# Performance work log

Measured on AMD Instinct MI355X. Metric: run time of the kernel, lower is better.

Reference implementation:

```python
import jax, jax.numpy as jnp
import numpy as np

B, S, D, F, E, TOP_K = 2, 2048, 1024, 2048, 8, 2


def setup_inputs() -> dict:
    key = jax.random.key(0)
    k0, k1, k2, k3 = jax.random.split(key, 4)
    return {
        "hidden_states": jax.random.normal(k0, (B, S, D), jnp.float32),
        "gate_w": jax.random.normal(k1, (E, D), jnp.float32) * 0.02,   # torch Linear weight [out=E, in=D]
        "w1": jax.random.normal(k2, (E, D, F), jnp.float32) * 0.02,    # per-expert up-proj
        "w2": jax.random.normal(k3, (E, F, D), jnp.float32) * 0.02,    # per-expert down-proj
    }


def reference(hidden_states, gate_w, w1, w2):
    b, s, d = hidden_states.shape
    e = gate_w.shape[0]
    x = hidden_states.reshape(-1, d)                 # [T, D]
    t = x.shape[0]
    router_logits = x @ gate_w.T                     # [T, E]
    # softmax in fp32 as in original, then renormalized top-k weights
    probs = jax.nn.softmax(router_logits.astype(jnp.float32), axis=-1)
    topw, sel = jax.lax.top_k(probs, TOP_K)          # [T, K]
    topw = topw / jnp.sum(topw, axis=-1, keepdims=True)
    topw = topw.astype(x.dtype)
    # dense combine weights: zero for unselected experts (top_k indices are distinct)
    combine = jnp.zeros((t, e), x.dtype).at[jnp.arange(t)[:, None], sel].add(topw)  # [T, E]
    out = jnp.zeros_like(x)
    for ei in range(e):  # small fixed expert count
        h = jax.nn.silu(x @ w1[ei]) @ w2[ei]         # [T, D]
        out = out + combine[:, ei:ei + 1] * h
    return out.reshape(b, s, d), router_logits
```

## Files before the change

### kernel.cpp

```cpp
#include <hip/hip_runtime.h>
#include <hip/hip_bf16.h>
#include <math.h>

#define Tt 4096
#define Dd 1024
#define Ff 2048
#define Ee 8

typedef unsigned short u16;
typedef short bf16x8 __attribute__((ext_vector_type(8)));
typedef float f32x4 __attribute__((ext_vector_type(4)));

__device__ __forceinline__ u16 f2bf(float f) {
  union { float f; unsigned u; } v; v.f = f;
  unsigned r = v.u + 0x7fffu + ((v.u >> 16) & 1u);
  return (u16)(r >> 16);
}

__device__ __forceinline__ void gload16(const void* g, void* l) {
  __builtin_amdgcn_global_load_lds(
      (const __attribute__((address_space(1))) unsigned int*)g,
      (__attribute__((address_space(3))) unsigned int*)l, 16, 0, 0);
}

__global__ __launch_bounds__(256) void router_kernel(
    const float* __restrict__ x, const float* __restrict__ gw,
    float* __restrict__ logits, u16* __restrict__ xb)
{
  int t = blockIdx.x * 4 + (threadIdx.x >> 6);
  int lane = threadIdx.x & 63;
  const float* xr = x + (size_t)t * Dd;
  float xv[16];
#pragma unroll
  for (int i = 0; i < 4; ++i) {
    float4 v = *reinterpret_cast<const float4*>(xr + lane * 16 + i * 4);
    xv[i*4+0] = v.x; xv[i*4+1] = v.y; xv[i*4+2] = v.z; xv[i*4+3] = v.w;
  }
  if (xb) {
#pragma unroll
    for (int i = 0; i < 4; ++i) {
      ushort4 b;
      b.x = f2bf(xv[i*4+0]); b.y = f2bf(xv[i*4+1]);
      b.z = f2bf(xv[i*4+2]); b.w = f2bf(xv[i*4+3]);
      *reinterpret_cast<ushort4*>(xb + (size_t)t * Dd + lane * 16 + i * 4) = b;
    }
  }
#pragma unroll
  for (int e = 0; e < Ee; ++e) {
    const float* gr = gw + (size_t)e * Dd + lane * 16;
    float s = 0.f;
#pragma unroll
    for (int i = 0; i < 4; ++i) {
      float4 g = *reinterpret_cast<const float4*>(gr + i * 4);
      s += xv[i*4+0]*g.x + xv[i*4+1]*g.y + xv[i*4+2]*g.z + xv[i*4+3]*g.w;
    }
#pragma unroll
    for (int o = 32; o > 0; o >>= 1) s += __shfl_xor(s, o);
    if (lane == 0) logits[(size_t)t * Ee + e] = s;
  }
}

__global__ __launch_bounds__(256) void build_kernel(
    const float* __restrict__ logits, int* __restrict__ meta,
    int* __restrict__ list, float* __restrict__ wgt)
{
  __shared__ int hist[8], cur[8];
  const int tid = threadIdx.x;
  const int lane = tid & 63;
  if (tid < 8) hist[tid] = 0;
  __syncthreads();
  for (int it = 0; it < Tt / 256; ++it) {
    int t = it * 256 + tid;
    float4 lo = *reinterpret_cast<const float4*>(logits + (size_t)t * 8);
    float4 hi = *reinterpret_cast<const float4*>(logits + (size_t)t * 8 + 4);
    float s[8] = {lo.x, lo.y, lo.z, lo.w, hi.x, hi.y, hi.z, hi.w};
    int i1 = 0; float m1 = s[0];
#pragma unroll
    for (int e = 1; e < 8; ++e) if (s[e] > m1) { m1 = s[e]; i1 = e; }
    int i2 = -1; float m2 = -__builtin_inff();
#pragma unroll
    for (int e = 0; e < 8; ++e) if (e != i1 && s[e] > m2) { m2 = s[e]; i2 = e; }
#pragma unroll
    for (int k = 0; k < 2; ++k) {
      int gg = k ? i2 : i1;
      unsigned long long m = ~0ull;
#pragma unroll
      for (int b = 0; b < 3; ++b) {
        unsigned long long vb = __ballot((gg >> b) & 1);
        m &= ((gg >> b) & 1) ? vb : ~vb;
      }
      int rank = __popcll(m & ((1ull << lane) - 1));
      if (rank == 0) atomicAdd(&hist[gg], __popcll(m));
    }
  }
  __syncthreads();
  if (tid == 0) {
    int sacc = 0;
    for (int g = 0; g < 8; ++g) {
      meta[g] = hist[g];
      meta[32 + g] = sacc;
      cur[g] = sacc;
      sacc += hist[g];
    }
  }
  __syncthreads();
  for (int it = 0; it < Tt / 256; ++it) {
    int t = it * 256 + tid;
    float4 lo = *reinterpret_cast<const float4*>(logits + (size_t)t * 8);
    float4 hi = *reinterpret_cast<const float4*>(logits + (size_t)t * 8 + 4);
    float s[8] = {lo.x, lo.y, lo.z, lo.w, hi.x, hi.y, hi.z, hi.w};
    int i1 = 0; float m1 = s[0];
#pragma unroll
    for (int e = 1; e < 8; ++e) if (s[e] > m1) { m1 = s[e]; i1 = e; }
    int i2 = -1; float m2 = -__builtin_inff();
#pragma unroll
    for (int e = 0; e < 8; ++e) if (e != i1 && s[e] > m2) { m2 = s[e]; i2 = e; }
    float wa = 1.f / (1.f + expf(m2 - m1));
#pragma unroll
    for (int k = 0; k < 2; ++k) {
      int gg = k ? i2 : i1;
      float w = k ? (1.f - wa) : wa;
      unsigned long long m = ~0ull;
#pragma unroll
      for (int b = 0; b < 3; ++b) {
        unsigned long long vb = __ballot((gg >> b) & 1);
        m &= ((gg >> b) & 1) ? vb : ~vb;
      }
      int rank = __popcll(m & ((1ull << lane) - 1));
      int ldr = __ffsll(m) - 1;
      int base = 0;
      if (rank == 0) base = atomicAdd(&cur[gg], __popcll(m));
      base = __shfl(base, ldr);
      list[base + rank] = t;
      wgt[base + rank] = w;
    }
  }
}

__global__ __launch_bounds__(256) void transpose_bf16_kernel(
    const float* __restrict__ in, u16* __restrict__ out, int R, int C)
{
  __shared__ u16 st[64][65];
  const size_t eoff = (size_t)blockIdx.z * R * C;
  const float* ip = in + eoff;
  u16* op = out + eoff;
  int r0 = blockIdx.y * 64, c0 = blockIdx.x * 64;
  int t = threadIdx.x;
  int rr = t >> 2;
  int cb = (t & 3) * 16;
#pragma unroll
  for (int i = 0; i < 4; ++i) {
    float4 v = *reinterpret_cast<const float4*>(ip + (size_t)(r0 + rr) * C + c0 + cb + i * 4);
    st[rr][cb + i*4 + 0] = f2bf(v.x);
    st[rr][cb + i*4 + 1] = f2bf(v.y);
    st[rr][cb + i*4 + 2] = f2bf(v.z);
    st[rr][cb + i*4 + 3] = f2bf(v.w);
  }
  __syncthreads();
#pragma unroll
  for (int i = 0; i < 4; ++i) {
    ushort4 b;
    b.x = st[cb + i*4 + 0][rr];
    b.y = st[cb + i*4 + 1][rr];
    b.z = st[cb + i*4 + 2][rr];
    b.w = st[cb + i*4 + 3][rr];
    *reinterpret_cast<ushort4*>(op + (size_t)(c0 + rr) * R + r0 + cb + i * 4) = b;
  }
}

template<int MODE, int N_, int K_>
__global__ __launch_bounds__(256) void gemm_g(
    const u16* __restrict__ Abase, const u16* __restrict__ Bbase,
    void* __restrict__ Cout, const int* __restrict__ meta,
    const int* __restrict__ list, const float* __restrict__ wgt)
{
  constexpr int NXc = N_ / 128;
  constexpr int NYc = 32;
  constexpr int CPX = NXc * NYc;
  constexpr int ABUF = 128 * 32;
  constexpr int NT  = K_ / 32;

  __shared__ u16 Al[3 * ABUF];
  __shared__ u16 Bl[3 * ABUF];

  const int orig = blockIdx.x + NXc * (blockIdx.y + NYc * blockIdx.z);
  const int swz  = (orig & 7) * CPX + (orig >> 3);
  const int bz   = swz / (NXc * NYc);
  const int rem  = swz - bz * (NXc * NYc);
  const int by   = rem / NXc;
  const int bx   = rem - by * NXc;

  const int e   = bz;
  const int cnt = meta[e];
  if (by * 128 >= cnt) return;
  const int off = meta[32 + e];

  const int tid  = threadIdx.x;
  const int lane = tid & 63;
  const int wave = tid >> 6;
  const int wr   = wave >> 1, wc = wave & 1;
  const int n0   = bx * 128;

  const int l4 = lane >> 2;
  const int kp = (((lane & 3) ^ ((lane >> 3) & 3))) * 8;

  const u16* aptr[2];
  int aoff[2];
#pragma unroll
  for (int c = 0; c < 2; ++c) {
    int chunk = wave * 2 + c;
    int row = chunk * 16 + l4;
    int i = by * 128 + row;
    if (i >= cnt) i = cnt - 1;
    int srow = (MODE == 0) ? list[off + i] : (off + i);
    aptr[c] = Abase + (size_t)srow * K_ + kp;
    aoff[c] = chunk * 512;
  }
  const u16* bptr[2];
  int boff[2];
#pragma unroll
  for (int c = 0; c < 2; ++c) {
    int chunk = wave * 2 + c;
    int row = chunk * 16 + l4;
    bptr[c] = Bbase + ((size_t)e * N_ + n0 + row) * K_ + kp;
    boff[c] = chunk * 512;
  }

  f32x4 acc[4][4] = {};
  const int r16 = lane & 15;
  const int kqs = (((lane >> 4) ^ ((lane >> 1) & 3))) * 8;

  u16 *a0 = Al, *a1 = Al + ABUF, *a2 = Al + 2 * ABUF;
  u16 *b0 = Bl, *b1 = Bl + ABUF, *b2 = Bl + 2 * ABUF;

#pragma unroll
  for (int c = 0; c < 2; ++c) { gload16(aptr[c], a0 + aoff[c]); gload16(bptr[c], b0 + boff[c]); }
#pragma unroll
  for (int c = 0; c < 2; ++c) { gload16(aptr[c] + 32, a1 + aoff[c]); gload16(bptr[c] + 32, b1 + boff[c]); }

  for (int t = 0; t < NT; ++t) {
    if (t + 1 < NT) asm volatile("s_waitcnt vmcnt(4)" ::: "memory");
    else            asm volatile("s_waitcnt vmcnt(0)" ::: "memory");
    __builtin_amdgcn_s_barrier();

    if (t + 2 < NT) {
      int k0 = (t + 2) * 32;
#pragma unroll
      for (int c = 0; c < 2; ++c) { gload16(aptr[c] + k0, a2 + aoff[c]); gload16(bptr[c] + k0, b2 + boff[c]); }
    }

    bf16x8 af[4], bfv[4];
#pragma unroll
    for (int m = 0; m < 4; ++m)
      af[m] = *reinterpret_cast<const bf16x8*>(&a0[(wr*64 + m*16 + r16) * 32 + kqs]);
#pragma unroll
    for (int n = 0; n < 4; ++n)
      bfv[n] = *reinterpret_cast<const bf16x8*>(&b0[(wc*64 + n*16 + r16) * 32 + kqs]);
    __builtin_amdgcn_s_setprio(1);
#pragma unroll
    for (int m = 0; m < 4; ++m)
#pragma unroll
      for (int n = 0; n < 4; ++n)
        acc[m][n] = __builtin_amdgcn_mfma_f32_16x16x32_bf16(af[m], bfv[n], acc[m][n], 0, 0, 0);
    __builtin_amdgcn_s_setprio(0);

    u16* ta = a0; a0 = a1; a1 = a2; a2 = ta;
    u16* tb = b0; b0 = b1; b1 = b2; b2 = tb;
  }

  const int colb = n0 + wc * 64 + r16;
  const int rb4  = wr * 64 + ((lane >> 4) << 2);
#pragma unroll
  for (int m = 0; m < 4; ++m) {
#pragma unroll
    for (int r = 0; r < 4; ++r) {
      int i = by * 128 + rb4 + m * 16 + r;
      if (i >= cnt) continue;
      if (MODE == 0) {
        u16* hp = (u16*)Cout + (size_t)(off + i) * N_;
#pragma unroll
        for (int n = 0; n < 4; ++n) {
          float v = acc[m][n][r];
          v = v / (1.f + expf(-v));
          hp[colb + n * 16] = f2bf(v);
        }
      } else {
        int   tok = list[off + i];
        float w   = wgt[off + i];
        float* o = (float*)Cout + (size_t)tok * N_;
#pragma unroll
        for (int n = 0; n < 4; ++n)
          atomicAdd(&o[colb + n * 16], w * acc[m][n][r]);
      }
    }
  }
}

__global__ __launch_bounds__(256) void combine_kernel(
    const float* __restrict__ logits, float* __restrict__ combine)
{
  int t = blockIdx.x * 256 + threadIdx.x;
  if (t >= Tt) return;
  float4 lo = *reinterpret_cast<const float4*>(logits + (size_t)t * 8);
  float4 hi = *reinterpret_cast<const float4*>(logits + (size_t)t * 8 + 4);
  float s[8] = {lo.x, lo.y, lo.z, lo.w, hi.x, hi.y, hi.z, hi.w};
  int i1 = 0; float m1 = s[0];
#pragma unroll
  for (int e = 1; e < 8; ++e) if (s[e] > m1) { m1 = s[e]; i1 = e; }
  int i2 = -1; float m2 = -__builtin_inff();
#pragma unroll
  for (int e = 0; e < 8; ++e) if (e != i1 && s[e] > m2) { m2 = s[e]; i2 = e; }
  float wa = 1.f / (1.f + expf(m2 - m1));
#pragma unroll
  for (int e = 0; e < 8; ++e)
    combine[(size_t)t * 8 + e] = (e == i1) ? wa : ((e == i2) ? (1.f - wa) : 0.f);
}

template<int MODE, int N_, int K_>
__global__ __launch_bounds__(256) void gemm_dense(
    const float* __restrict__ A, const float* __restrict__ Bg,
    float* __restrict__ C, const float* __restrict__ combine,
    int expert, int first)
{
  constexpr int BM = 128, BN = 128, BK = 32, LDT = 40;
  __shared__ u16 Al[BM * LDT];
  __shared__ u16 Bl[BN * LDT];
  const int tid  = threadIdx.x;
  const int lane = tid & 63;
  const int wave = tid >> 6;
  const int wr = wave >> 1, wc = wave & 1;
  const int m0 = blockIdx.y * BM;
  const int n0 = blockIdx.x * BN;
  f32x4 acc[4][4] = {};
  for (int k0 = 0; k0 < K_; k0 += BK) {
#pragma unroll
    for (int i = 0; i < 4; ++i) {
      int f = tid + 256 * i;
      int row = f >> 3;
      int c4 = (f & 7) << 2;
      float4 v = *reinterpret_cast<const float4*>(A + (size_t)(m0 + row) * K_ + k0 + c4);
      ushort4 b;
      b.x = f2bf(v.x); b.y = f2bf(v.y); b.z = f2bf(v.z); b.w = f2bf(v.w);
      *reinterpret_cast<ushort4*>(&Al[row * LDT + c4]) = b;
    }
    {
      int n  = tid & 127;
      int kb = (tid >> 7) << 4;
      const float* bp = Bg + (size_t)(k0 + kb) * N_ + n0 + n;
      u16 tmp[16];
#pragma unroll
      for (int kk = 0; kk < 16; ++kk)
        tmp[kk] = f2bf(bp[(size_t)kk * N_]);
      u16* p = &Bl[n * LDT + kb];
#pragma unroll
      for (int i = 0; i < 4; ++i) {
        ushort4 b;
        b.x = tmp[i*4+0]; b.y = tmp[i*4+1]; b.z = tmp[i*4+2]; b.w = tmp[i*4+3];
        *reinterpret_cast<ushort4*>(p + i * 4) = b;
      }
    }
    __syncthreads();
    bf16x8 af[4], bfr[4];
    const int kq  = (lane >> 4) << 3;
    const int r16 = lane & 15;
#pragma unroll
    for (int m = 0; m < 4; ++m)
      af[m] = *reinterpret_cast<const bf16x8*>(&Al[(wr*64 + m*16 + r16) * LDT + kq]);
#pragma unroll
    for (int n = 0; n < 4; ++n)
      bfr[n] = *reinterpret_cast<const bf16x8*>(&Bl[(wc*64 + n*16 + r16) * LDT + kq]);
#pragma unroll
    for (int m = 0; m < 4; ++m)
#pragma unroll
      for (int n = 0; n < 4; ++n)
        acc[m][n] = __builtin_amdgcn_mfma_f32_16x16x32_bf16(af[m], bfr[n], acc[m][n], 0, 0, 0);
    __syncthreads();
  }
  const int col0 = n0 + wc * 64 + (lane & 15);
  const int rbs  = m0 + wr * 64 + ((lane >> 4) << 2);
#pragma unroll
  for (int m = 0; m < 4; ++m) {
#pragma unroll
    for (int r = 0; r < 4; ++r) {
      int row = rbs + m * 16 + r;
      if (MODE == 0) {
#pragma unroll
        for (int n = 0; n < 4; ++n) {
          float v = acc[m][n][r];
          v = v / (1.f + expf(-v));
          C[(size_t)row * N_ + col0 + n * 16] = v;
        }
      } else {
        float w = combine[(size_t)row * Ee + expert];
        if (first) {
#pragma unroll
          for (int n = 0; n < 4; ++n)
            C[(size_t)row * N_ + col0 + n * 16] = w * acc[m][n][r];
        } else {
#pragma unroll
          for (int n = 0; n < 4; ++n)
            C[(size_t)row * N_ + col0 + n * 16] += w * acc[m][n][r];
        }
      }
    }
  }
}

extern "C" void kernel_launch(void* const* d_in, const int* in_sizes, int n_in,
                              void* d_out, int out_size, void* d_ws, size_t ws_size,
                              hipStream_t stream)
{
  const float* x  = (const float*)d_in[0];
  const float* gw = (const float*)d_in[1];
  const float* w1 = (const float*)d_in[2];
  const float* w2 = (const float*)d_in[3];
  float* out    = (float*)d_out;
  float* logits = out + (size_t)Tt * Dd;

  int*   meta = (int*)d_ws;
  int*   list = (int*)((char*)d_ws + 256);
  float* wgt  = (float*)((char*)d_ws + 256 + 32768);
  u16*   xb   = (u16*)((char*)d_ws + 262144);
  u16*   h1   = (u16*)((char*)d_ws + 262144 + 8388608);
  u16*   wT   = (u16*)((char*)d_ws + 262144 + 8388608 + 33554432);
  const size_t NEED = 262144ull + 8388608ull + 33554432ull + 33554432ull;

  if (ws_size >= NEED) {
    router_kernel<<<Tt / 4, 256, 0, stream>>>(x, gw, logits, xb);
    hipMemsetAsync(out, 0, (size_t)Tt * Dd * sizeof(float), stream);
    build_kernel<<<1, 256, 0, stream>>>(logits, meta, list, wgt);
    transpose_bf16_kernel<<<dim3(Ff/64, Dd/64, Ee), 256, 0, stream>>>(w1, wT, Dd, Ff);
    gemm_g<0, Ff, Dd><<<dim3(Ff/128, 32, 8), 256, 0, stream>>>(xb, wT, h1, meta, list, wgt);
    transpose_bf16_kernel<<<dim3(Dd/64, Ff/64, Ee), 256, 0, stream>>>(w2, wT, Ff, Dd);
    gemm_g<1, Dd, Ff><<<dim3(Dd/128, 32, 8), 256, 0, stream>>>(h1, wT, out, meta, list, wgt);
  } else {
    float* combine = (float*)d_ws;
    float* h1d     = combine + (size_t)Tt * Ee;
    router_kernel<<<Tt / 4, 256, 0, stream>>>(x, gw, logits, nullptr);
    combine_kernel<<<Tt / 256, 256, 0, stream>>>(logits, combine);
    size_t cb = (size_t)Tt * Ee * sizeof(float);
    size_t avail = ws_size > cb ? (ws_size - cb) : 0;
    long maxrows = (long)(avail / ((size_t)Ff * sizeof(float)));
    int chunk = (maxrows >= Tt) ? Tt : (int)((maxrows / 128) * 128);
    if (chunk < 128) chunk = 128;
    for (int c0 = 0; c0 < Tt; c0 += chunk) {
      int rows = (Tt - c0) < chunk ? (Tt - c0) : chunk;
      for (int e = 0; e < Ee; ++e) {
        gemm_dense<0, Ff, Dd><<<dim3(Ff/128, rows/128), 256, 0, stream>>>(
            x + (size_t)c0 * Dd, w1 + (size_t)e * Dd * Ff, h1d, nullptr, e, 0);
        gemm_dense<1, Dd, Ff><<<dim3(Dd/128, rows/128), 256, 0, stream>>>(
            h1d, w2 + (size_t)e * Ff * Dd, out + (size_t)c0 * Dd,
            combine + (size_t)c0 * Ee, e, (e == 0) ? 1 : 0);
      }
    }
  }
}
```

Before: 207.2 us.

## Enlarge grouped GEMM tile to 256x128 and split-K the down-projection

The grouped expert GEMMs now use a 256-row by 128-column block tile, with each wave covering 64 rows across all 128 columns, so B tiles are reused over more rows and fewer blocks are launched. The down-projection GEMM also splits K in two, with each half atomically accumulating into the output, to restore the parallelism lost from the larger tile. The accumulator grows to 4x8 per wave under a 2-blocks-per-CU launch bound, which raises register pressure and LDS use. The split doubles the fp32 atomic traffic on the output.

```diff
diff --git a/kernel.cpp b/kernel.cpp
--- a/kernel.cpp
+++ b/kernel.cpp
@@ -168,20 +168,23 @@
   }
 }
 
-template<int MODE, int N_, int K_>
-__global__ __launch_bounds__(256) void gemm_g(
+template<int MODE, int N_, int K_, int KSPLIT>
+__global__ __launch_bounds__(256, 2) void gemm_g(
     const u16* __restrict__ Abase, const u16* __restrict__ Bbase,
     void* __restrict__ Cout, const int* __restrict__ meta,
     const int* __restrict__ list, const float* __restrict__ wgt)
 {
+  constexpr int BM  = 256;
   constexpr int NXc = N_ / 128;
-  constexpr int NYc = 32;
-  constexpr int CPX = NXc * NYc;
-  constexpr int ABUF = 128 * 32;
-  constexpr int NT  = K_ / 32;
+  constexpr int NYc = 16;
+  constexpr int CPX = NXc * NYc * KSPLIT;
+  constexpr int ABUF = BM * 32;
+  constexpr int BBUF = 128 * 32;
+  constexpr int KLOC = K_ / KSPLIT;
+  constexpr int NT  = KLOC / 32;
 
   __shared__ u16 Al[3 * ABUF];
-  __shared__ u16 Bl[3 * ABUF];
+  __shared__ u16 Bl[3 * BBUF];
 
   const int orig = blockIdx.x + NXc * (blockIdx.y + NYc * blockIdx.z);
   const int swz  = (orig & 7) * CPX + (orig >> 3);
@@ -190,77 +193,84 @@
   const int by   = rem / NXc;
   const int bx   = rem - by * NXc;
 
-  const int e   = bz;
+  const int e   = bz / KSPLIT;
+  const int kh  = bz - e * KSPLIT;
   const int cnt = meta[e];
-  if (by * 128 >= cnt) return;
+  if (by * BM >= cnt) return;
   const int off = meta[32 + e];
+  const int kbase = kh * KLOC;
 
   const int tid  = threadIdx.x;
   const int lane = tid & 63;
   const int wave = tid >> 6;
-  const int wr   = wave >> 1, wc = wave & 1;
   const int n0   = bx * 128;
 
   const int l4 = lane >> 2;
   const int kp = (((lane & 3) ^ ((lane >> 3) & 3))) * 8;
 
-  const u16* aptr[2];
-  int aoff[2];
+  const u16* aptr[4];
+  int aoff[4];
+#pragma unroll
+  for (int c = 0; c < 4; ++c) {
+    int chunk = wave * 4 + c;
+    int rw = chunk * 16 + l4;
+    int i = by * BM + rw;
+    if (i >= cnt) i = cnt - 1;
+    int srow = (MODE == 0) ? list[off + i] : (off + i);
+    aptr[c] = Abase + (size_t)srow * K_ + kbase + kp;
+    aoff[c] = chunk * 512;
+  }
+  const u16* bptr[2];
+  int boff[2];
 #pragma unroll
   for (int c = 0; c < 2; ++c) {
     int chunk = wave * 2 + c;
-    int row = chunk * 16 + l4;
-    int i = by * 128 + row;
-    if (i >= cnt) i = cnt - 1;
-    int srow = (MODE == 0) ? list[off + i] : (off + i);
-    aptr[c] = Abase + (size_t)srow * K_ + kp;
-    aoff[c] = chunk * 512;
-  }
-  const u16* bptr[2];
-  int boff[2];
-#pragma unroll
-  for (int c = 0; c < 2; ++c) {
-    int chunk = wave * 2 + c;
-    int row = chunk * 16 + l4;
-    bptr[c] = Bbase + ((size_t)e * N_ + n0 + row) * K_ + kp;
+    int rw = chunk * 16 + l4;
+    bptr[c] = Bbase + ((size_t)e * N_ + n0 + rw) * K_ + kbase + kp;
     boff[c] = chunk * 512;
   }
 
-  f32x4 acc[4][4] = {};
+  f32x4 acc[4][8] = {};
   const int r16 = lane & 15;
   const int kqs = (((lane >> 4) ^ ((lane >> 1) & 3))) * 8;
 
   u16 *a0 = Al, *a1 = Al + ABUF, *a2 = Al + 2 * ABUF;
-  u16 *b0 = Bl, *b1 = Bl + ABUF, *b2 = Bl + 2 * ABUF;
-
-#pragma unroll
-  for (int c = 0; c < 2; ++c) { gload16(aptr[c], a0 + aoff[c]); gload16(bptr[c], b0 + boff[c]); }
-#pragma unroll
-  for (int c = 0; c < 2; ++c) { gload16(aptr[c] + 32, a1 + aoff[c]); gload16(bptr[c] + 32, b1 + boff[c]); }
+  u16 *b0 = Bl, *b1 = Bl + BBUF, *b2 = Bl + 2 * BBUF;
+
+#pragma unroll
+  for (int c = 0; c < 4; ++c) gload16(aptr[c], a0 + aoff[c]);
+#pragma unroll
+  for (int c = 0; c < 2; ++c) gload16(bptr[c], b0 + boff[c]);
+#pragma unroll
+  for (int c = 0; c < 4; ++c) gload16(aptr[c] + 32, a1 + aoff[c]);
+#pragma unroll
+  for (int c = 0; c < 2; ++c) gload16(bptr[c] + 32, b1 + boff[c]);
 
   for (int t = 0; t < NT; ++t) {
-    if (t + 1 < NT) asm volatile("s_waitcnt vmcnt(4)" ::: "memory");
+    if (t + 1 < NT) asm volatile("s_waitcnt vmcnt(6)" ::: "memory");
     else            asm volatile("s_waitcnt vmcnt(0)" ::: "memory");
     __builtin_amdgcn_s_barrier();
 
     if (t + 2 < NT) {
       int k0 = (t + 2) * 32;
 #pragma unroll
-      for (int c = 0; c < 2; ++c) { gload16(aptr[c] + k0, a2 + aoff[c]); gload16(bptr[c] + k0, b2 + boff[c]); }
-    }
-
-    bf16x8 af[4], bfv[4];
+      for (int c = 0; c < 4; ++c) gload16(aptr[c] + k0, a2 + aoff[c]);
+#pragma unroll
+      for (int c = 0; c < 2; ++c) gload16(bptr[c] + k0, b2 + boff[c]);
+    }
+
+    bf16x8 af[4], bfv[8];
 #pragma unroll
     for (int m = 0; m < 4; ++m)
-      af[m] = *reinterpret_cast<const bf16x8*>(&a0[(wr*64 + m*16 + r16) * 32 + kqs]);
-#pragma unroll
-    for (int n = 0; n < 4; ++n)
-      bfv[n] = *reinterpret_cast<const bf16x8*>(&b0[(wc*64 + n*16 + r16) * 32 + kqs]);
+      af[m] = *reinterpret_cast<const bf16x8*>(&a0[(wave*64 + m*16 + r16) * 32 + kqs]);
+#pragma unroll
+    for (int n = 0; n < 8; ++n)
+      bfv[n] = *reinterpret_cast<const bf16x8*>(&b0[(n*16 + r16) * 32 + kqs]);
     __builtin_amdgcn_s_setprio(1);
 #pragma unroll
     for (int m = 0; m < 4; ++m)
 #pragma unroll
-      for (int n = 0; n < 4; ++n)
+      for (int n = 0; n < 8; ++n)
         acc[m][n] = __builtin_amdgcn_mfma_f32_16x16x32_bf16(af[m], bfv[n], acc[m][n], 0, 0, 0);
     __builtin_amdgcn_s_setprio(0);
 
@@ -268,29 +278,28 @@
     u16* tb = b0; b0 = b1; b1 = b2; b2 = tb;
   }
 
-  const int colb = n0 + wc * 64 + r16;
-  const int rb4  = wr * 64 + ((lane >> 4) << 2);
+  const int rb4 = wave * 64 + ((lane >> 4) << 2);
 #pragma unroll
   for (int m = 0; m < 4; ++m) {
 #pragma unroll
     for (int r = 0; r < 4; ++r) {
-      int i = by * 128 + rb4 + m * 16 + r;
+      int i = by * BM + rb4 + m * 16 + r;
       if (i >= cnt) continue;
       if (MODE == 0) {
         u16* hp = (u16*)Cout + (size_t)(off + i) * N_;
 #pragma unroll
-        for (int n = 0; n < 4; ++n) {
+        for (int n = 0; n < 8; ++n) {
           float v = acc[m][n][r];
           v = v / (1.f + expf(-v));
-          hp[colb + n * 16] = f2bf(v);
+          hp[n0 + n * 16 + r16] = f2bf(v);
         }
       } else {
         int   tok = list[off + i];
         float w   = wgt[off + i];
         float* o = (float*)Cout + (size_t)tok * N_;
 #pragma unroll
-        for (int n = 0; n < 4; ++n)
-          atomicAdd(&o[colb + n * 16], w * acc[m][n][r]);
+        for (int n = 0; n < 8; ++n)
+          atomicAdd(&o[n0 + n * 16 + r16], w * acc[m][n][r]);
       }
     }
   }
@@ -430,9 +439,9 @@
     hipMemsetAsync(out, 0, (size_t)Tt * Dd * sizeof(float), stream);
     build_kernel<<<1, 256, 0, stream>>>(logits, meta, list, wgt);
     transpose_bf16_kernel<<<dim3(Ff/64, Dd/64, Ee), 256, 0, stream>>>(w1, wT, Dd, Ff);
-    gemm_g<0, Ff, Dd><<<dim3(Ff/128, 32, 8), 256, 0, stream>>>(xb, wT, h1, meta, list, wgt);
+    gemm_g<0, Ff, Dd, 1><<<dim3(Ff/128, 16, 8), 256, 0, stream>>>(xb, wT, h1, meta, list, wgt);
     transpose_bf16_kernel<<<dim3(Dd/64, Ff/64, Ee), 256, 0, stream>>>(w2, wT, Ff, Dd);
-    gemm_g<1, Dd, Ff><<<dim3(Dd/128, 32, 8), 256, 0, stream>>>(h1, wT, out, meta, list, wgt);
+    gemm_g<1, Dd, Ff, 2><<<dim3(Dd/128, 16, 16), 256, 0, stream>>>(h1, wT, out, meta, list, wgt);
   } else {
     float* combine = (float*)d_ws;
     float* h1d     = combine + (size_t)Tt * Ee;
```

New measurement: 253.5 us. +22.3%, slower.

## Make grouped MoE GEMM persistent over row tiles and swizzle transpose blocks

Applied to the files above, without the earlier changes.

The grouped expert GEMMs now launch 12 row-tile slots per expert instead of 32. Each block loops over row tiles with a stride of 12 until it has covered that expert's token count, with a barrier between tiles so the shared-memory buffers can be reused. Most of the 32 row slots in the old grid returned immediately, so this cuts launch overhead and empty blocks, but large experts become serial within a block. The weight transpose kernel also gets the same XCD-style block-index swizzle used by the GEMM, to spread experts across dies.

```diff
diff --git a/kernel.cpp b/kernel.cpp
--- a/kernel.cpp
+++ b/kernel.cpp
@@ -141,10 +141,20 @@
     const float* __restrict__ in, u16* __restrict__ out, int R, int C)
 {
   __shared__ u16 st[64][65];
-  const size_t eoff = (size_t)blockIdx.z * R * C;
+  const int gx = gridDim.x, gy = gridDim.y;
+  const int plane = gx * gy;
+  const int cpx = plane;
+  const int orig = blockIdx.x + gx * (blockIdx.y + gy * blockIdx.z);
+  const int swz  = (orig & 7) * cpx + (orig >> 3);
+  const int ez   = swz / plane;
+  const int rem  = swz - ez * plane;
+  const int byy  = rem / gx;
+  const int bxx  = rem - byy * gx;
+
+  const size_t eoff = (size_t)ez * R * C;
   const float* ip = in + eoff;
   u16* op = out + eoff;
-  int r0 = blockIdx.y * 64, c0 = blockIdx.x * 64;
+  int r0 = byy * 64, c0 = bxx * 64;
   int t = threadIdx.x;
   int rr = t >> 2;
   int cb = (t & 3) * 16;
@@ -175,7 +185,7 @@
     const int* __restrict__ list, const float* __restrict__ wgt)
 {
   constexpr int NXc = N_ / 128;
-  constexpr int NYc = 32;
+  constexpr int NYc = 12;
   constexpr int CPX = NXc * NYc;
   constexpr int ABUF = 128 * 32;
   constexpr int NT  = K_ / 32;
@@ -185,14 +195,13 @@
 
   const int orig = blockIdx.x + NXc * (blockIdx.y + NYc * blockIdx.z);
   const int swz  = (orig & 7) * CPX + (orig >> 3);
-  const int bz   = swz / (NXc * NYc);
-  const int rem  = swz - bz * (NXc * NYc);
-  const int by   = rem / NXc;
-  const int bx   = rem - by * NXc;
+  const int bz   = swz / CPX;
+  const int rem  = swz - bz * CPX;
+  const int by0  = rem / NXc;
+  const int bx   = rem - by0 * NXc;
 
   const int e   = bz;
   const int cnt = meta[e];
-  if (by * 128 >= cnt) return;
   const int off = meta[32 + e];
 
   const int tid  = threadIdx.x;
@@ -203,96 +212,98 @@
 
   const int l4 = lane >> 2;
   const int kp = (((lane & 3) ^ ((lane >> 3) & 3))) * 8;
-
-  const u16* aptr[2];
-  int aoff[2];
-#pragma unroll
-  for (int c = 0; c < 2; ++c) {
-    int chunk = wave * 2 + c;
-    int row = chunk * 16 + l4;
-    int i = by * 128 + row;
-    if (i >= cnt) i = cnt - 1;
-    int srow = (MODE == 0) ? list[off + i] : (off + i);
-    aptr[c] = Abase + (size_t)srow * K_ + kp;
-    aoff[c] = chunk * 512;
-  }
-  const u16* bptr[2];
-  int boff[2];
-#pragma unroll
-  for (int c = 0; c < 2; ++c) {
-    int chunk = wave * 2 + c;
-    int row = chunk * 16 + l4;
-    bptr[c] = Bbase + ((size_t)e * N_ + n0 + row) * K_ + kp;
-    boff[c] = chunk * 512;
-  }
-
-  f32x4 acc[4][4] = {};
   const int r16 = lane & 15;
   const int kqs = (((lane >> 4) ^ ((lane >> 1) & 3))) * 8;
 
-  u16 *a0 = Al, *a1 = Al + ABUF, *a2 = Al + 2 * ABUF;
-  u16 *b0 = Bl, *b1 = Bl + ABUF, *b2 = Bl + 2 * ABUF;
-
-#pragma unroll
-  for (int c = 0; c < 2; ++c) { gload16(aptr[c], a0 + aoff[c]); gload16(bptr[c], b0 + boff[c]); }
-#pragma unroll
-  for (int c = 0; c < 2; ++c) { gload16(aptr[c] + 32, a1 + aoff[c]); gload16(bptr[c] + 32, b1 + boff[c]); }
-
-  for (int t = 0; t < NT; ++t) {
-    if (t + 1 < NT) asm volatile("s_waitcnt vmcnt(4)" ::: "memory");
-    else            asm volatile("s_waitcnt vmcnt(0)" ::: "memory");
-    __builtin_amdgcn_s_barrier();
-
-    if (t + 2 < NT) {
-      int k0 = (t + 2) * 32;
-#pragma unroll
-      for (int c = 0; c < 2; ++c) { gload16(aptr[c] + k0, a2 + aoff[c]); gload16(bptr[c] + k0, b2 + boff[c]); }
-    }
-
-    bf16x8 af[4], bfv[4];
-#pragma unroll
-    for (int m = 0; m < 4; ++m)
-      af[m] = *reinterpret_cast<const bf16x8*>(&a0[(wr*64 + m*16 + r16) * 32 + kqs]);
-#pragma unroll
-    for (int n = 0; n < 4; ++n)
-      bfv[n] = *reinterpret_cast<const bf16x8*>(&b0[(wc*64 + n*16 + r16) * 32 + kqs]);
-    __builtin_amdgcn_s_setprio(1);
-#pragma unroll
-    for (int m = 0; m < 4; ++m)
+  for (int by = by0; by * 128 < cnt; by += NYc) {
+    const u16* aptr[2];
+    int aoff[2];
+#pragma unroll
+    for (int c = 0; c < 2; ++c) {
+      int chunk = wave * 2 + c;
+      int rw = chunk * 16 + l4;
+      int i = by * 128 + rw;
+      if (i >= cnt) i = cnt - 1;
+      int srow = (MODE == 0) ? list[off + i] : (off + i);
+      aptr[c] = Abase + (size_t)srow * K_ + kp;
+      aoff[c] = chunk * 512;
+    }
+    const u16* bptr[2];
+    int boff[2];
+#pragma unroll
+    for (int c = 0; c < 2; ++c) {
+      int chunk = wave * 2 + c;
+      int rw = chunk * 16 + l4;
+      bptr[c] = Bbase + ((size_t)e * N_ + n0 + rw) * K_ + kp;
+      boff[c] = chunk * 512;
+    }
+
+    f32x4 acc[4][4] = {};
+    u16 *a0 = Al, *a1 = Al + ABUF, *a2 = Al + 2 * ABUF;
+    u16 *b0 = Bl, *b1 = Bl + ABUF, *b2 = Bl + 2 * ABUF;
+
+#pragma unroll
+    for (int c = 0; c < 2; ++c) { gload16(aptr[c], a0 + aoff[c]); gload16(bptr[c], b0 + boff[c]); }
+#pragma unroll
+    for (int c = 0; c < 2; ++c) { gload16(aptr[c] + 32, a1 + aoff[c]); gload16(bptr[c] + 32, b1 + boff[c]); }
+
+    for (int t = 0; t < NT; ++t) {
+      if (t + 1 < NT) asm volatile("s_waitcnt vmcnt(4)" ::: "memory");
+      else            asm volatile("s_waitcnt vmcnt(0)" ::: "memory");
+      __builtin_amdgcn_s_barrier();
+
+      if (t + 2 < NT) {
+        int k0 = (t + 2) * 32;
+#pragma unroll
+        for (int c = 0; c < 2; ++c) { gload16(aptr[c] + k0, a2 + aoff[c]); gload16(bptr[c] + k0, b2 + boff[c]); }
+      }
+
+      bf16x8 af[4], bfv[4];
+#pragma unroll
+      for (int m = 0; m < 4; ++m)
+        af[m] = *reinterpret_cast<const bf16x8*>(&a0[(wr*64 + m*16 + r16) * 32 + kqs]);
 #pragma unroll
       for (int n = 0; n < 4; ++n)
-        acc[m][n] = __builtin_amdgcn_mfma_f32_16x16x32_bf16(af[m], bfv[n], acc[m][n], 0, 0, 0);
-    __builtin_amdgcn_s_setprio(0);
-
-    u16* ta = a0; a0 = a1; a1 = a2; a2 = ta;
-    u16* tb = b0; b0 = b1; b1 = b2; b2 = tb;
-  }
-
-  const int colb = n0 + wc * 64 + r16;
-  const int rb4  = wr * 64 + ((lane >> 4) << 2);
-#pragma unroll
-  for (int m = 0; m < 4; ++m) {
-#pragma unroll
-    for (int r = 0; r < 4; ++r) {
-      int i = by * 128 + rb4 + m * 16 + r;
-      if (i >= cnt) continue;
-      if (MODE == 0) {
-        u16* hp = (u16*)Cout + (size_t)(off + i) * N_;
-#pragma unroll
-        for (int n = 0; n < 4; ++n) {
-          float v = acc[m][n][r];
-          v = v / (1.f + expf(-v));
-          hp[colb + n * 16] = f2bf(v);
+        bfv[n] = *reinterpret_cast<const bf16x8*>(&b0[(wc*64 + n*16 + r16) * 32 + kqs]);
+      __builtin_amdgcn_s_setprio(1);
+#pragma unroll
+      for (int m = 0; m < 4; ++m)
+#pragma unroll
+        for (int n = 0; n < 4; ++n)
+          acc[m][n] = __builtin_amdgcn_mfma_f32_16x16x32_bf16(af[m], bfv[n], acc[m][n], 0, 0, 0);
+      __builtin_amdgcn_s_setprio(0);
+
+      u16* ta = a0; a0 = a1; a1 = a2; a2 = ta;
+      u16* tb = b0; b0 = b1; b1 = b2; b2 = tb;
+    }
+
+    const int colb = n0 + wc * 64 + r16;
+    const int rb4  = wr * 64 + ((lane >> 4) << 2);
+#pragma unroll
+    for (int m = 0; m < 4; ++m) {
+#pragma unroll
+      for (int r = 0; r < 4; ++r) {
+        int i = by * 128 + rb4 + m * 16 + r;
+        if (i >= cnt) continue;
+        if (MODE == 0) {
+          u16* hp = (u16*)Cout + (size_t)(off + i) * N_;
+#pragma unroll
+          for (int n = 0; n < 4; ++n) {
+            float v = acc[m][n][r];
+            v = v / (1.f + expf(-v));
+            hp[colb + n * 16] = f2bf(v);
+          }
+        } else {
+          int   tok = list[off + i];
+          float w   = wgt[off + i];
+          float* o = (float*)Cout + (size_t)tok * N_;
+#pragma unroll
+          for (int n = 0; n < 4; ++n)
+            atomicAdd(&o[colb + n * 16], w * acc[m][n][r]);
         }
-      } else {
-        int   tok = list[off + i];
-        float w   = wgt[off + i];
-        float* o = (float*)Cout + (size_t)tok * N_;
-#pragma unroll
-        for (int n = 0; n < 4; ++n)
-          atomicAdd(&o[colb + n * 16], w * acc[m][n][r]);
-      }
-    }
+      }
+    }
+    __syncthreads();
   }
 }
 
@@ -430,9 +441,9 @@
     hipMemsetAsync(out, 0, (size_t)Tt * Dd * sizeof(float), stream);
     build_kernel<<<1, 256, 0, stream>>>(logits, meta, list, wgt);
     transpose_bf16_kernel<<<dim3(Ff/64, Dd/64, Ee), 256, 0, stream>>>(w1, wT, Dd, Ff);
-    gemm_g<0, Ff, Dd><<<dim3(Ff/128, 32, 8), 256, 0, stream>>>(xb, wT, h1, meta, list, wgt);
+    gemm_g<0, Ff, Dd><<<dim3(Ff/128, 12, 8), 256, 0, stream>>>(xb, wT, h1, meta, list, wgt);
     transpose_bf16_kernel<<<dim3(Dd/64, Ff/64, Ee), 256, 0, stream>>>(w2, wT, Ff, Dd);
-    gemm_g<1, Dd, Ff><<<dim3(Dd/128, 32, 8), 256, 0, stream>>>(h1, wT, out, meta, list, wgt);
+    gemm_g<1, Dd, Ff><<<dim3(Dd/128, 12, 8), 256, 0, stream>>>(h1, wT, out, meta, list, wgt);
   } else {
     float* combine = (float*)d_ws;
     float* h1d     = combine + (size_t)Tt * Ee;
```

Result: slower. 282.9 us (+36.5%).

## Fuse router with w1 transpose and overlap w2 transpose with first GEMM

Applied to the files above, without the earlier changes.

Merges the router and the w1 fp32-to-bf16 transpose into one launch of heterogeneous blocks. It also merges the first grouped GEMM with the w2 transpose, using a separate workspace buffer so both can run concurrently. This is meant to cut launch gaps and fill idle CUs: many first-GEMM blocks exit early because of per-expert token counts, and transpose blocks can occupy those CUs. The cost is an extra 32MB of workspace, and the fused GEMM kernel's LDS footprint applies to the transpose blocks too. If the workspace is too small, it falls back to the old sequence.

```diff
diff --git a/kernel.cpp b/kernel.cpp
--- a/kernel.cpp
+++ b/kernel.cpp
@@ -23,12 +23,11 @@
       (__attribute__((address_space(3))) unsigned int*)l, 16, 0, 0);
 }
 
-__global__ __launch_bounds__(256) void router_kernel(
-    const float* __restrict__ x, const float* __restrict__ gw,
+__device__ __forceinline__ void router_body(
+    int t, int tid, const float* __restrict__ x, const float* __restrict__ gw,
     float* __restrict__ logits, u16* __restrict__ xb)
 {
-  int t = blockIdx.x * 4 + (threadIdx.x >> 6);
-  int lane = threadIdx.x & 63;
+  int lane = tid & 63;
   const float* xr = x + (size_t)t * Dd;
   float xv[16];
 #pragma unroll
@@ -58,6 +57,228 @@
     for (int o = 32; o > 0; o >>= 1) s += __shfl_xor(s, o);
     if (lane == 0) logits[(size_t)t * Ee + e] = s;
   }
+}
+
+__device__ __forceinline__ void transpose_tile(
+    const float* __restrict__ ip, u16* __restrict__ op, int R, int C,
+    int r0, int c0, int tid, u16 st[][65])
+{
+  int rr = tid >> 2;
+  int cb = (tid & 3) * 16;
+#pragma unroll
+  for (int i = 0; i < 4; ++i) {
+    float4 v = *reinterpret_cast<const float4*>(ip + (size_t)(r0 + rr) * C + c0 + cb + i * 4);
+    st[rr][cb + i*4 + 0] = f2bf(v.x);
+    st[rr][cb + i*4 + 1] = f2bf(v.y);
+    st[rr][cb + i*4 + 2] = f2bf(v.z);
+    st[rr][cb + i*4 + 3] = f2bf(v.w);
+  }
+  __syncthreads();
+#pragma unroll
+  for (int i = 0; i < 4; ++i) {
+    ushort4 b;
+    b.x = st[cb + i*4 + 0][rr];
+    b.y = st[cb + i*4 + 1][rr];
+    b.z = st[cb + i*4 + 2][rr];
+    b.w = st[cb + i*4 + 3][rr];
+    *reinterpret_cast<ushort4*>(op + (size_t)(c0 + rr) * R + r0 + cb + i * 4) = b;
+  }
+}
+
+template<int MODE, int N_, int K_>
+__device__ __forceinline__ void gemm_body(
+    int orig, u16* __restrict__ Al, u16* __restrict__ Bl,
+    const u16* __restrict__ Abase, const u16* __restrict__ Bbase,
+    void* __restrict__ Cout, const int* __restrict__ meta,
+    const int* __restrict__ list, const float* __restrict__ wgt)
+{
+  constexpr int NXc = N_ / 128;
+  constexpr int NYc = 32;
+  constexpr int CPX = NXc * NYc;
+  constexpr int ABUF = 128 * 32;
+  constexpr int NT  = K_ / 32;
+
+  const int swz  = (orig & 7) * CPX + (orig >> 3);
+  const int bz   = swz / CPX;
+  const int rem  = swz - bz * CPX;
+  const int by   = rem / NXc;
+  const int bx   = rem - by * NXc;
+
+  const int e   = bz;
+  const int cnt = meta[e];
+  if (by * 128 >= cnt) return;
+  const int off = meta[32 + e];
+
+  const int tid  = threadIdx.x;
+  const int lane = tid & 63;
+  const int wave = tid >> 6;
+  const int wr   = wave >> 1, wc = wave & 1;
+  const int n0   = bx * 128;
+
+  const int l4 = lane >> 2;
+  const int kp = (((lane & 3) ^ ((lane >> 3) & 3))) * 8;
+
+  const u16* aptr[2];
+  int aoff[2];
+#pragma unroll
+  for (int c = 0; c < 2; ++c) {
+    int chunk = wave * 2 + c;
+    int row = chunk * 16 + l4;
+    int i = by * 128 + row;
+    if (i >= cnt) i = cnt - 1;
+    int srow = (MODE == 0) ? list[off + i] : (off + i);
+    aptr[c] = Abase + (size_t)srow * K_ + kp;
+    aoff[c] = chunk * 512;
+  }
+  const u16* bptr[2];
+  int boff[2];
+#pragma unroll
+  for (int c = 0; c < 2; ++c) {
+    int chunk = wave * 2 + c;
+    int row = chunk * 16 + l4;
+    bptr[c] = Bbase + ((size_t)e * N_ + n0 + row) * K_ + kp;
+    boff[c] = chunk * 512;
+  }
+
+  f32x4 acc[4][4] = {};
+  const int r16 = lane & 15;
+  const int kqs = (((lane >> 4) ^ ((lane >> 1) & 3))) * 8;
+
+  u16 *a0 = Al, *a1 = Al + ABUF, *a2 = Al + 2 * ABUF;
+  u16 *b0 = Bl, *b1 = Bl + ABUF, *b2 = Bl + 2 * ABUF;
+
+#pragma unroll
+  for (int c = 0; c < 2; ++c) { gload16(aptr[c], a0 + aoff[c]); gload16(bptr[c], b0 + boff[c]); }
+#pragma unroll
+  for (int c = 0; c < 2; ++c) { gload16(aptr[c] + 32, a1 + aoff[c]); gload16(bptr[c] + 32, b1 + boff[c]); }
+
+  for (int t = 0; t < NT; ++t) {
+    if (t + 1 < NT) asm volatile("s_waitcnt vmcnt(4)" ::: "memory");
+    else            asm volatile("s_waitcnt vmcnt(0)" ::: "memory");
+    __builtin_amdgcn_s_barrier();
+
+    if (t + 2 < NT) {
+      int k0 = (t + 2) * 32;
+#pragma unroll
+      for (int c = 0; c < 2; ++c) { gload16(aptr[c] + k0, a2 + aoff[c]); gload16(bptr[c] + k0, b2 + boff[c]); }
+    }
+
+    bf16x8 af[4], bfv[4];
+#pragma unroll
+    for (int m = 0; m < 4; ++m)
+      af[m] = *reinterpret_cast<const bf16x8*>(&a0[(wr*64 + m*16 + r16) * 32 + kqs]);
+#pragma unroll
+    for (int n = 0; n < 4; ++n)
+      bfv[n] = *reinterpret_cast<const bf16x8*>(&b0[(wc*64 + n*16 + r16) * 32 + kqs]);
+    __builtin_amdgcn_s_setprio(1);
+#pragma unroll
+    for (int m = 0; m < 4; ++m)
+#pragma unroll
+      for (int n = 0; n < 4; ++n)
+        acc[m][n] = __builtin_amdgcn_mfma_f32_16x16x32_bf16(af[m], bfv[n], acc[m][n], 0, 0, 0);
+    __builtin_amdgcn_s_setprio(0);
+
+    u16* ta = a0; a0 = a1; a1 = a2; a2 = ta;
+    u16* tb = b0; b0 = b1; b1 = b2; b2 = tb;
+  }
+
+  const int colb = n0 + wc * 64 + r16;
+  const int rb4  = wr * 64 + ((lane >> 4) << 2);
+#pragma unroll
+  for (int m = 0; m < 4; ++m) {
+#pragma unroll
+    for (int r = 0; r < 4; ++r) {
+      int i = by * 128 + rb4 + m * 16 + r;
+      if (i >= cnt) continue;
+      if (MODE == 0) {
+        u16* hp = (u16*)Cout + (size_t)(off + i) * N_;
+#pragma unroll
+        for (int n = 0; n < 4; ++n) {
+          float v = acc[m][n][r];
+          v = v / (1.f + expf(-v));
+          hp[colb + n * 16] = f2bf(v);
+        }
+      } else {
+        int   tok = list[off + i];
+        float w   = wgt[off + i];
+        float* o = (float*)Cout + (size_t)tok * N_;
+#pragma unroll
+        for (int n = 0; n < 4; ++n)
+          atomicAdd(&o[colb + n * 16], w * acc[m][n][r]);
+      }
+    }
+  }
+}
+
+__global__ __launch_bounds__(256) void router_kernel(
+    const float* __restrict__ x, const float* __restrict__ gw,
+    float* __restrict__ logits, u16* __restrict__ xb)
+{
+  router_body(blockIdx.x * 4 + (threadIdx.x >> 6), threadIdx.x, x, gw, logits, xb);
+}
+
+__global__ __launch_bounds__(256) void fuse1_kernel(
+    const float* __restrict__ x, const float* __restrict__ gw,
+    float* __restrict__ logits, u16* __restrict__ xb,
+    const float* __restrict__ w1, u16* __restrict__ w1T)
+{
+  __shared__ u16 st[64][65];
+  const int orig = blockIdx.x;
+  if (orig < 4096) {
+    int swz = (orig & 7) * 512 + (orig >> 3);
+    int e   = swz / 512;
+    int rem = swz - e * 512;
+    int by  = rem / 32, bx = rem - (rem / 32) * 32;
+    const size_t eo = (size_t)e * Dd * Ff;
+    transpose_tile(w1 + eo, w1T + eo, Dd, Ff, by * 64, bx * 64, threadIdx.x, st);
+  } else {
+    router_body((orig - 4096) * 4 + (threadIdx.x >> 6), threadIdx.x, x, gw, logits, xb);
+  }
+}
+
+__global__ __launch_bounds__(256) void fuse2_kernel(
+    const u16* __restrict__ Abase, const u16* __restrict__ Bbase,
+    void* __restrict__ Cout, const int* __restrict__ meta,
+    const int* __restrict__ list, const float* __restrict__ wgt,
+    const float* __restrict__ w2, u16* __restrict__ w2T)
+{
+  constexpr int ABUF = 128 * 32;
+  __shared__ u16 pool[6 * ABUF];
+  const int orig = blockIdx.x;
+  if (orig < 4096) {
+    gemm_body<0, Ff, Dd>(orig, pool, pool + 3 * ABUF, Abase, Bbase, Cout, meta, list, wgt);
+  } else {
+    int og  = orig - 4096;
+    int swz = (og & 7) * 512 + (og >> 3);
+    int e   = swz / 512;
+    int rem = swz - e * 512;
+    int byy = rem / 16, bxx = rem - (rem / 16) * 16;
+    const size_t eo = (size_t)e * Ff * Dd;
+    transpose_tile(w2 + eo, w2T + eo, Ff, Dd, byy * 64, bxx * 64, threadIdx.x,
+                   reinterpret_cast<u16(*)[65]>(pool));
+  }
+}
+
+template<int MODE, int N_, int K_>
+__global__ __launch_bounds__(256) void gemm_g(
+    const u16* __restrict__ Abase, const u16* __restrict__ Bbase,
+    void* __restrict__ Cout, const int* __restrict__ meta,
+    const int* __restrict__ list, const float* __restrict__ wgt)
+{
+  constexpr int ABUF = 128 * 32;
+  __shared__ u16 Al[3 * ABUF];
+  __shared__ u16 Bl[3 * ABUF];
+  const int orig = blockIdx.x + (N_ / 128) * (blockIdx.y + 32 * blockIdx.z);
+  gemm_body<MODE, N_, K_>(orig, Al, Bl, Abase, Bbase, Cout, meta, list, wgt);
+}
+
+__global__ __launch_bounds__(256) void transpose_bf16_kernel(
+    const float* __restrict__ in, u16* __restrict__ out, int R, int C)
+{
+  __shared__ u16 st[64][65];
+  const size_t eoff = (size_t)blockIdx.z * R * C;
+  transpose_tile(in + eoff, out + eoff, R, C, blockIdx.y * 64, blockIdx.x * 64,
+                 threadIdx.x, st);
 }
 
 __global__ __launch_bounds__(256) void build_kernel(
@@ -137,165 +358,6 @@
   }
 }
 
-__global__ __launch_bounds__(256) void transpose_bf16_kernel(
-    const float* __restrict__ in, u16* __restrict__ out, int R, int C)
-{
-  __shared__ u16 st[64][65];
-  const size_t eoff = (size_t)blockIdx.z * R * C;
-  const float* ip = in + eoff;
-  u16* op = out + eoff;
-  int r0 = blockIdx.y * 64, c0 = blockIdx.x * 64;
-  int t = threadIdx.x;
-  int rr = t >> 2;
-  int cb = (t & 3) * 16;
-#pragma unroll
-  for (int i = 0; i < 4; ++i) {
-    float4 v = *reinterpret_cast<const float4*>(ip + (size_t)(r0 + rr) * C + c0 + cb + i * 4);
-    st[rr][cb + i*4 + 0] = f2bf(v.x);
-    st[rr][cb + i*4 + 1] = f2bf(v.y);
-    st[rr][cb + i*4 + 2] = f2bf(v.z);
-    st[rr][cb + i*4 + 3] = f2bf(v.w);
-  }
-  __syncthreads();
-#pragma unroll
-  for (int i = 0; i < 4; ++i) {
-    ushort4 b;
-    b.x = st[cb + i*4 + 0][rr];
-    b.y = st[cb + i*4 + 1][rr];
-    b.z = st[cb + i*4 + 2][rr];
-    b.w = st[cb + i*4 + 3][rr];
-    *reinterpret_cast<ushort4*>(op + (size_t)(c0 + rr) * R + r0 + cb + i * 4) = b;
-  }
-}
-
-template<int MODE, int N_, int K_>
-__global__ __launch_bounds__(256) void gemm_g(
-    const u16* __restrict__ Abase, const u16* __restrict__ Bbase,
-    void* __restrict__ Cout, const int* __restrict__ meta,
-    const int* __restrict__ list, const float* __restrict__ wgt)
-{
-  constexpr int NXc = N_ / 128;
-  constexpr int NYc = 32;
-  constexpr int CPX = NXc * NYc;
-  constexpr int ABUF = 128 * 32;
-  constexpr int NT  = K_ / 32;
-
-  __shared__ u16 Al[3 * ABUF];
-  __shared__ u16 Bl[3 * ABUF];
-
-  const int orig = blockIdx.x + NXc * (blockIdx.y + NYc * blockIdx.z);
-  const int swz  = (orig & 7) * CPX + (orig >> 3);
-  const int bz   = swz / (NXc * NYc);
-  const int rem  = swz - bz * (NXc * NYc);
-  const int by   = rem / NXc;
-  const int bx   = rem - by * NXc;
-
-  const int e   = bz;
-  const int cnt = meta[e];
-  if (by * 128 >= cnt) return;
-  const int off = meta[32 + e];
-
-  const int tid  = threadIdx.x;
-  const int lane = tid & 63;
-  const int wave = tid >> 6;
-  const int wr   = wave >> 1, wc = wave & 1;
-  const int n0   = bx * 128;
-
-  const int l4 = lane >> 2;
-  const int kp = (((lane & 3) ^ ((lane >> 3) & 3))) * 8;
-
-  const u16* aptr[2];
-  int aoff[2];
-#pragma unroll
-  for (int c = 0; c < 2; ++c) {
-    int chunk = wave * 2 + c;
-    int row = chunk * 16 + l4;
-    int i = by * 128 + row;
-    if (i >= cnt) i = cnt - 1;
-    int srow = (MODE == 0) ? list[off + i] : (off + i);
-    aptr[c] = Abase + (size_t)srow * K_ + kp;
-    aoff[c] = chunk * 512;
-  }
-  const u16* bptr[2];
-  int boff[2];
-#pragma unroll
-  for (int c = 0; c < 2; ++c) {
-    int chunk = wave * 2 + c;
-    int row = chunk * 16 + l4;
-    bptr[c] = Bbase + ((size_t)e * N_ + n0 + row) * K_ + kp;
-    boff[c] = chunk * 512;
-  }
-
-  f32x4 acc[4][4] = {};
-  const int r16 = lane & 15;
-  const int kqs = (((lane >> 4) ^ ((lane >> 1) & 3))) * 8;
-
-  u16 *a0 = Al, *a1 = Al + ABUF, *a2 = Al + 2 * ABUF;
-  u16 *b0 = Bl, *b1 = Bl + ABUF, *b2 = Bl + 2 * ABUF;
-
-#pragma unroll
-  for (int c = 0; c < 2; ++c) { gload16(aptr[c], a0 + aoff[c]); gload16(bptr[c], b0 + boff[c]); }
-#pragma unroll
-  for (int c = 0; c < 2; ++c) { gload16(aptr[c] + 32, a1 + aoff[c]); gload16(bptr[c] + 32, b1 + boff[c]); }
-
-  for (int t = 0; t < NT; ++t) {
-    if (t + 1 < NT) asm volatile("s_waitcnt vmcnt(4)" ::: "memory");
-    else            asm volatile("s_waitcnt vmcnt(0)" ::: "memory");
-    __builtin_amdgcn_s_barrier();
-
-    if (t + 2 < NT) {
-      int k0 = (t + 2) * 32;
-#pragma unroll
-      for (int c = 0; c < 2; ++c) { gload16(aptr[c] + k0, a2 + aoff[c]); gload16(bptr[c] + k0, b2 + boff[c]); }
-    }
-
-    bf16x8 af[4], bfv[4];
-#pragma unroll
-    for (int m = 0; m < 4; ++m)
-      af[m] = *reinterpret_cast<const bf16x8*>(&a0[(wr*64 + m*16 + r16) * 32 + kqs]);
-#pragma unroll
-    for (int n = 0; n < 4; ++n)
-      bfv[n] = *reinterpret_cast<const bf16x8*>(&b0[(wc*64 + n*16 + r16) * 32 + kqs]);
-    __builtin_amdgcn_s_setprio(1);
-#pragma unroll
-    for (int m = 0; m < 4; ++m)
-#pragma unroll
-      for (int n = 0; n < 4; ++n)
-        acc[m][n] = __builtin_amdgcn_mfma_f32_16x16x32_bf16(af[m], bfv[n], acc[m][n], 0, 0, 0);
-    __builtin_amdgcn_s_setprio(0);
-
-    u16* ta = a0; a0 = a1; a1 = a2; a2 = ta;
-    u16* tb = b0; b0 = b1; b1 = b2; b2 = tb;
-  }
-
-  const int colb = n0 + wc * 64 + r16;
-  const int rb4  = wr * 64 + ((lane >> 4) << 2);
-#pragma unroll
-  for (int m = 0; m < 4; ++m) {
-#pragma unroll
-    for (int r = 0; r < 4; ++r) {
-      int i = by * 128 + rb4 + m * 16 + r;
-      if (i >= cnt) continue;
-      if (MODE == 0) {
-        u16* hp = (u16*)Cout + (size_t)(off + i) * N_;
-#pragma unroll
-        for (int n = 0; n < 4; ++n) {
-          float v = acc[m][n][r];
-          v = v / (1.f + expf(-v));
-          hp[colb + n * 16] = f2bf(v);
-        }
-      } else {
-        int   tok = list[off + i];
-        float w   = wgt[off + i];
-        float* o = (float*)Cout + (size_t)tok * N_;
-#pragma unroll
-        for (int n = 0; n < 4; ++n)
-          atomicAdd(&o[colb + n * 16], w * acc[m][n][r]);
-      }
-    }
-  }
-}
-
 __global__ __launch_bounds__(256) void combine_kernel(
     const float* __restrict__ logits, float* __restrict__ combine)
 {
@@ -422,17 +484,23 @@
   float* wgt  = (float*)((char*)d_ws + 256 + 32768);
   u16*   xb   = (u16*)((char*)d_ws + 262144);
   u16*   h1   = (u16*)((char*)d_ws + 262144 + 8388608);
-  u16*   wT   = (u16*)((char*)d_ws + 262144 + 8388608 + 33554432);
-  const size_t NEED = 262144ull + 8388608ull + 33554432ull + 33554432ull;
-
-  if (ws_size >= NEED) {
-    router_kernel<<<Tt / 4, 256, 0, stream>>>(x, gw, logits, xb);
+  u16*   wA   = (u16*)((char*)d_ws + 262144 + 8388608 + 33554432);
+  u16*   wB   = (u16*)((char*)d_ws + 262144 + 8388608 + 2*33554432ull);
+  const size_t NEED_B = 262144ull + 8388608ull + 33554432ull + 33554432ull;
+  const size_t NEED_A = NEED_B + 33554432ull;
+
+  if (ws_size >= NEED_B) {
+    fuse1_kernel<<<5120, 256, 0, stream>>>(x, gw, logits, xb, w1, wA);
     hipMemsetAsync(out, 0, (size_t)Tt * Dd * sizeof(float), stream);
     build_kernel<<<1, 256, 0, stream>>>(logits, meta, list, wgt);
-    transpose_bf16_kernel<<<dim3(Ff/64, Dd/64, Ee), 256, 0, stream>>>(w1, wT, Dd, Ff);
-    gemm_g<0, Ff, Dd><<<dim3(Ff/128, 32, 8), 256, 0, stream>>>(xb, wT, h1, meta, list, wgt);
-    transpose_bf16_kernel<<<dim3(Dd/64, Ff/64, Ee), 256, 0, stream>>>(w2, wT, Ff, Dd);
-    gemm_g<1, Dd, Ff><<<dim3(Dd/128, 32, 8), 256, 0, stream>>>(h1, wT, out, meta, list, wgt);
+    if (ws_size >= NEED_A) {
+      fuse2_kernel<<<8192, 256, 0, stream>>>(xb, wA, h1, meta, list, wgt, w2, wB);
+      gemm_g<1, Dd, Ff><<<dim3(Dd/128, 32, 8), 256, 0, stream>>>(h1, wB, out, meta, list, wgt);
+    } else {
+      gemm_g<0, Ff, Dd><<<dim3(Ff/128, 32, 8), 256, 0, stream>>>(xb, wA, h1, meta, list, wgt);
+      transpose_bf16_kernel<<<dim3(Dd/64, Ff/64, Ee), 256, 0, stream>>>(w2, wA, Ff, Dd);
+      gemm_g<1, Dd, Ff><<<dim3(Dd/128, 32, 8), 256, 0, stream>>>(h1, wA, out, meta, list, wgt);
+    }
   } else {
     float* combine = (float*)d_ws;
     float* h1d     = combine + (size_t)Tt * Ee;
```

After: 195.4 us. -5.7%, faster.
